# Performance work log

Measured on AMD Instinct MI355X. Metric: run time of the kernel, lower is better.

Reference implementation:

```python
import jax, jax.numpy as jnp
import numpy as np


def setup_inputs() -> dict:
    key = jax.random.key(0)
    kq, kk, kv, km = jax.random.split(key, 4)
    B, H, S, D = 8, 16, 1024, 64
    Q = jax.random.normal(kq, (B, H, S, D), dtype=jnp.float32)
    K = jax.random.normal(kk, (B, H, S, D), dtype=jnp.float32)
    V = jax.random.normal(kv, (B, H, S, D), dtype=jnp.float32)
    # True means masked, per torch masked_fill_ semantics
    attn_mask = jax.random.randint(km, (B, 1, S, S), 0, 2).astype(bool)
    return {"Q": Q, "K": K, "V": V, "attn_mask": attn_mask}


def reference(Q, K, V, attn_mask):
    # Attention(Q,K,V) = softmax(QK^T / sqrt(d_k)) V, with masked scores
    # set to 1e-9 (faithful to the original's masked_fill_(mask, 1e-09)).
    d_k = Q.shape[-1]
    scores = jnp.einsum('bhqd,bhkd->bhqk', Q, K) / jnp.sqrt(jnp.float32(d_k))
    scores = jnp.where(attn_mask, jnp.asarray(1e-9, scores.dtype), scores)
    attn = jax.nn.softmax(scores, axis=-1)          # [B,H,S,S]
    context = jnp.einsum('bhqk,bhkd->bhqd', attn, V)  # [B,H,S,D]
    return (context, attn)
```

## Files before the change

### kernel.cpp

```cpp
#include <hip/hip_runtime.h>
#include <hip/hip_bf16.h>

typedef __attribute__((ext_vector_type(4))) float f32x4;
typedef __attribute__((ext_vector_type(8))) short bf16x8;
typedef __attribute__((ext_vector_type(4))) int   i32x4;
typedef __attribute__((ext_vector_type(4))) unsigned u32x4;

#define S_LEN 1024
#define DQ    64
#define VSTR  266
#define PSTR  264
#define CSTR  68

__device__ __forceinline__ unsigned pk2(float a, float b) {
    union { __hip_bfloat162 h; unsigned u; } v;
    v.h = __float22bfloat162_rn(make_float2(a, b));
    return v.u;
}

__device__ __forceinline__ bf16x8 pack8(float4 a, float4 b) {
    union { bf16x8 v; unsigned u[4]; } r;
    r.u[0] = pk2(a.x, a.y); r.u[1] = pk2(a.z, a.w);
    r.u[2] = pk2(b.x, b.y); r.u[3] = pk2(b.z, b.w);
    return r.v;
}

__device__ __forceinline__ bf16x8 ld_frag2(const unsigned short* p) {
    union { bf16x8 v; unsigned u[4]; } r;
    r.u[0] = *(const unsigned*)(p);
    r.u[1] = *(const unsigned*)(p + 2);
    r.u[2] = *(const unsigned*)(p + 16);
    r.u[3] = *(const unsigned*)(p + 18);
    return r.v;
}

__device__ __forceinline__ float bflo(unsigned u) { union { unsigned x; float f; } v; v.x = u << 16;         return v.f; }
__device__ __forceinline__ float bfhi(unsigned u) { union { unsigned x; float f; } v; v.x = u & 0xffff0000u; return v.f; }

__global__ __launch_bounds__(256) void pack_mask(const int* __restrict__ Mg,
                                                 unsigned long long* __restrict__ Pk) {
    const int gw   = (int)((blockIdx.x * 256 + threadIdx.x) >> 6);
    const int lane = threadIdx.x & 63;
#pragma unroll 4
    for (int j = 0; j < 32; ++j) {
        const size_t g = ((size_t)gw * 32 + j) * 64 + lane;
        const int m = __builtin_nontemporal_load(Mg + g);
        const unsigned long long bal = __ballot(m != 0);
        if (lane == 0) Pk[(size_t)gw * 32 + j] = bal;
    }
}

template <int PACKED>
__global__ __launch_bounds__(1024, 8) void attn_fused(
    const float* __restrict__ Qg, const float* __restrict__ Kg,
    const float* __restrict__ Vg, const int* __restrict__ Mg,
    const unsigned* __restrict__ Mb,
    float* __restrict__ Og, float* __restrict__ Ag)
{
    const int tid  = threadIdx.x;
    const int lane = tid & 63;
    const int wid  = tid >> 6;
    const int l15  = lane & 15;
    const int lg   = lane >> 4;
    const int wc   = wid >> 1;
    const int wr   = wid & 1;

    const int raw  = blockIdx.x;
    const int xcd  = raw & 7;
    const int slot = raw >> 3;
    const int bh   = xcd * 16 + (slot >> 5);
    const int qt   = slot & 31;
    const int b    = bh >> 4;

    const size_t kvbase = (size_t)bh * (S_LEN * DQ);
    const float* Qp = Qg + kvbase + (size_t)qt * (32 * DQ);
    const float* Kp = Kg + kvbase;
    const float* Vp = Vg + kvbase;
    float*       Ap = Ag + (size_t)bh * (size_t)(S_LEN * S_LEN) + (size_t)(qt * 32) * S_LEN;
    float*       Op = Og + kvbase + (size_t)qt * (32 * DQ);

    __shared__ __align__(16) unsigned char smem[32 * PSTR * 2 + DQ * VSTR * 2];
    unsigned short* Pt  = (unsigned short*)smem;
    float*          red = (float*)smem;
    float*          Cx  = (float*)smem;
    unsigned short* Vt  = (unsigned short*)(smem + 32 * PSTR * 2);

    const int qrow = wr * 16 + l15;

    unsigned mwd[4];
    if (PACKED) {
        const unsigned* mw = Mb + ((size_t)b * S_LEN + qt * 32 + qrow) * 32 + wc;
#pragma unroll
        for (int i = 0; i < 4; ++i) mwd[i] = mw[i * 8];
    }

    bf16x8 aq0, aq1;
    {
        const float* qr = Qp + (size_t)qrow * DQ + lg * 4;
        aq0 = pack8(*(const float4*)(qr),      *(const float4*)(qr + 16));
        aq1 = pack8(*(const float4*)(qr + 32), *(const float4*)(qr + 48));
    }

    f32x4 sc[8];
#pragma unroll
    for (int t = 0; t < 8; ++t) sc[t] = (f32x4){0.f, 0.f, 0.f, 0.f};

#pragma unroll
    for (int i = 0; i < 4; ++i)
#pragma unroll
        for (int h = 0; h < 2; ++h) {
            const float* krow = Kp + (size_t)(i * 256 + wc * 32 + h * 16 + l15) * DQ + lg * 4;
            bf16x8 k0 = pack8(*(const float4*)(krow),      *(const float4*)(krow + 16));
            bf16x8 k1 = pack8(*(const float4*)(krow + 32), *(const float4*)(krow + 48));
            f32x4 acc = sc[i * 2 + h];
            acc = __builtin_amdgcn_mfma_f32_16x16x32_bf16(k0, aq0, acc, 0, 0, 0);
            acc = __builtin_amdgcn_mfma_f32_16x16x32_bf16(k1, aq1, acc, 0, 0, 0);
            sc[i * 2 + h] = acc;
        }

    if (PACKED) {
#pragma unroll
        for (int i = 0; i < 4; ++i)
#pragma unroll
            for (int h = 0; h < 2; ++h) {
                const int t = i * 2 + h;
#pragma unroll
                for (int r = 0; r < 4; ++r)
                    sc[t][r] = ((mwd[i] >> (h * 16 + lg * 4 + r)) & 1u) ? 1e-9f
                                                                        : sc[t][r] * 0.125f;
            }
    } else {
        const int* mrow = Mg + (size_t)b * (size_t)(S_LEN * S_LEN)
                        + (size_t)(qt * 32 + qrow) * S_LEN + wc * 32 + lg * 4;
#pragma unroll
        for (int i = 0; i < 4; ++i)
#pragma unroll
            for (int h = 0; h < 2; ++h) {
                const i32x4 m4 = *(const i32x4*)(mrow + i * 256 + h * 16);
                const int t = i * 2 + h;
#pragma unroll
                for (int r = 0; r < 4; ++r)
                    sc[t][r] = m4[r] ? 1e-9f : sc[t][r] * 0.125f;
            }
    }

    float rmax = sc[0][0];
#pragma unroll
    for (int t = 0; t < 8; ++t)
#pragma unroll
        for (int r = 0; r < 4; ++r) rmax = fmaxf(rmax, sc[t][r]);
    rmax = fmaxf(rmax, __shfl_xor(rmax, 16));
    rmax = fmaxf(rmax, __shfl_xor(rmax, 32));
    __syncthreads();
    if (lane < 16) red[qrow * 8 + wc] = rmax;
    __syncthreads();
    {
        const f32x4 a = *(const f32x4*)(red + qrow * 8);
        const f32x4 bq = *(const f32x4*)(red + qrow * 8 + 4);
        rmax = fmaxf(fmaxf(fmaxf(a[0], a[1]), fmaxf(a[2], a[3])),
                     fmaxf(fmaxf(bq[0], bq[1]), fmaxf(bq[2], bq[3])));
    }

    float rsum = 0.f;
#pragma unroll
    for (int t = 0; t < 8; ++t)
#pragma unroll
        for (int r = 0; r < 4; ++r) {
            const float p = __expf(sc[t][r] - rmax);
            sc[t][r] = p;
            rsum += p;
        }
    rsum += __shfl_xor(rsum, 16);
    rsum += __shfl_xor(rsum, 32);
    __syncthreads();
    if (lane < 16) red[qrow * 8 + wc] = rsum;
    __syncthreads();
    float rinv;
    {
        const f32x4 a = *(const f32x4*)(red + qrow * 8);
        const f32x4 bq = *(const f32x4*)(red + qrow * 8 + 4);
        rinv = 1.0f / ((a[0] + a[1] + a[2] + a[3]) + (bq[0] + bq[1] + bq[2] + bq[3]));
    }
#pragma unroll
    for (int t = 0; t < 8; ++t)
#pragma unroll
        for (int r = 0; r < 4; ++r) sc[t][r] *= rinv;

    bf16x8 paf[4];
#pragma unroll
    for (int i = 0; i < 4; ++i) {
        union { bf16x8 v; unsigned u[4]; } pa;
        pa.u[0] = pk2(sc[i * 2][0],     sc[i * 2][1]);
        pa.u[1] = pk2(sc[i * 2][2],     sc[i * 2][3]);
        pa.u[2] = pk2(sc[i * 2 + 1][0], sc[i * 2 + 1][1]);
        pa.u[3] = pk2(sc[i * 2 + 1][2], sc[i * 2 + 1][3]);
        paf[i] = pa.v;
    }

    f32x4 co[4];
#pragma unroll
    for (int m = 0; m < 4; ++m) co[m] = (f32x4){0.f, 0.f, 0.f, 0.f};

#pragma unroll
    for (int i = 0; i < 4; ++i) {
        __syncthreads();

        const float* vsrc = Vp + (size_t)i * (256 * DQ);
#pragma unroll
        for (int j = 0; j < 4; ++j) {
            const int f = (j * 1024 + tid) * 4;
            const float4 v4 = *(const float4*)(vsrc + f);
            const int k = f >> 6, d = f & 63;
            const unsigned u0 = pk2(v4.x, v4.y);
            const unsigned u1 = pk2(v4.z, v4.w);
            Vt[(d + 0) * VSTR + k] = (unsigned short)u0;
            Vt[(d + 1) * VSTR + k] = (unsigned short)(u0 >> 16);
            Vt[(d + 2) * VSTR + k] = (unsigned short)u1;
            Vt[(d + 3) * VSTR + k] = (unsigned short)(u1 >> 16);
        }

        {
            union { bf16x8 v; unsigned long long q[2]; } pa;
            pa.v = paf[i];
            unsigned short* prow = Pt + qrow * PSTR + wc * 32 + lg * 4;
            *(unsigned long long*)(prow)      = pa.q[0];
            *(unsigned long long*)(prow + 16) = pa.q[1];
        }
        __syncthreads();

        {
            const int row = tid >> 5, c8 = tid & 31;
            const u32x4 u = *(const u32x4*)(Pt + row * PSTR + c8 * 8);
            const f32x4 o0 = { bflo(u[0]), bfhi(u[0]), bflo(u[1]), bfhi(u[1]) };
            const f32x4 o1 = { bflo(u[2]), bfhi(u[2]), bflo(u[3]), bfhi(u[3]) };
            float* dst = Ap + (size_t)row * S_LEN + i * 256 + c8 * 8;
            __builtin_nontemporal_store(o0, (f32x4*)(dst));
            __builtin_nontemporal_store(o1, (f32x4*)(dst + 4));
        }

#pragma unroll
        for (int m = 0; m < 4; ++m) {
            const bf16x8 bv = ld_frag2(Vt + (size_t)(m * 16 + l15) * VSTR + wc * 32 + lg * 4);
            co[m] = __builtin_amdgcn_mfma_f32_16x16x32_bf16(paf[i], bv, co[m], 0, 0, 0);
        }
    }

    __syncthreads();
#pragma unroll
    for (int w = 0; w < 8; ++w) {
        if (wc == w) {
#pragma unroll
            for (int m = 0; m < 4; ++m)
#pragma unroll
                for (int r = 0; r < 4; ++r) {
                    float* p = Cx + (size_t)(wr * 16 + lg * 4 + r) * CSTR + m * 16 + l15;
                    if (w == 0) *p = co[m][r];
                    else        *p += co[m][r];
                }
        }
        __syncthreads();
    }

    if (tid < 512) {
        const int row = tid >> 4, col = (tid & 15) * 4;
        const f32x4 o = *(const f32x4*)(Cx + (size_t)row * CSTR + col);
        __builtin_nontemporal_store(o, (f32x4*)(Op + (size_t)row * DQ + col));
    }
}

extern "C" void kernel_launch(void* const* d_in, const int* in_sizes, int n_in,
                              void* d_out, int out_size, void* d_ws, size_t ws_size,
                              hipStream_t stream) {
    const float* Q = (const float*)d_in[0];
    const float* K = (const float*)d_in[1];
    const float* V = (const float*)d_in[2];
    const int*   M = (const int*)d_in[3];
    float* ctx  = (float*)d_out;
    float* attn = ctx + (size_t)8 * 16 * 1024 * 64;

    const size_t packed_bytes = (size_t)8 * 1024 * 1024 / 8;
    if (ws_size >= packed_bytes) {
        pack_mask<<<dim3(1024), dim3(256), 0, stream>>>(M, (unsigned long long*)d_ws);
        attn_fused<1><<<dim3(4096), dim3(1024), 0, stream>>>(
            Q, K, V, M, (const unsigned*)d_ws, ctx, attn);
    } else {
        attn_fused<0><<<dim3(4096), dim3(1024), 0, stream>>>(
            Q, K, V, M, nullptr, ctx, attn);
    }
}
```

Measured before the change: 399.5 us.

## Halve query tile to 16 rows, prefetch K/V in registers, tree-reduce context

Shrinks each block to 16 query rows with 8 waves (512 threads) and doubles the grid. K fragments are double-buffered in registers, and V chunks are prefetched before the softmax and between iterations, so global loads overlap compute. The serialized 8-step shared-memory context accumulation becomes a single write-then-sum reduction, and V fragments load as 64-bit reads with a new padding stride. The cost is that K and V are reloaded twice as often across blocks and register pressure rises.

```diff
diff --git a/kernel.cpp b/kernel.cpp
--- a/kernel.cpp
+++ b/kernel.cpp
@@ -8,9 +8,12 @@
 
 #define S_LEN 1024
 #define DQ    64
-#define VSTR  266
+#define QTL   16
+#define VSTR  268
 #define PSTR  264
 #define CSTR  68
+#define PT_BYTES (QTL * PSTR * 2)
+#define VT_BYTES (DQ * VSTR * 2)
 
 __device__ __forceinline__ unsigned pk2(float a, float b) {
     union { __hip_bfloat162 h; unsigned u; } v;
@@ -25,12 +28,10 @@
     return r.v;
 }
 
-__device__ __forceinline__ bf16x8 ld_frag2(const unsigned short* p) {
-    union { bf16x8 v; unsigned u[4]; } r;
-    r.u[0] = *(const unsigned*)(p);
-    r.u[1] = *(const unsigned*)(p + 2);
-    r.u[2] = *(const unsigned*)(p + 16);
-    r.u[3] = *(const unsigned*)(p + 18);
+__device__ __forceinline__ bf16x8 ld_frag64(const unsigned short* p) {
+    union { bf16x8 v; unsigned long long q[2]; } r;
+    r.q[0] = *(const unsigned long long*)(p);
+    r.q[1] = *(const unsigned long long*)(p + 16);
     return r.v;
 }
 
@@ -51,7 +52,7 @@
 }
 
 template <int PACKED>
-__global__ __launch_bounds__(1024, 8) void attn_fused(
+__global__ __launch_bounds__(512, 6) void attn_fused(
     const float* __restrict__ Qg, const float* __restrict__ Kg,
     const float* __restrict__ Vg, const int* __restrict__ Mg,
     const unsigned* __restrict__ Mb,
@@ -59,37 +60,36 @@
 {
     const int tid  = threadIdx.x;
     const int lane = tid & 63;
-    const int wid  = tid >> 6;
+    const int wc   = tid >> 6;
     const int l15  = lane & 15;
     const int lg   = lane >> 4;
-    const int wc   = wid >> 1;
-    const int wr   = wid & 1;
 
     const int raw  = blockIdx.x;
     const int xcd  = raw & 7;
     const int slot = raw >> 3;
-    const int bh   = xcd * 16 + (slot >> 5);
-    const int qt   = slot & 31;
+    const int bh   = xcd * 16 + (slot >> 6);
+    const int qt   = slot & 63;
     const int b    = bh >> 4;
 
     const size_t kvbase = (size_t)bh * (S_LEN * DQ);
-    const float* Qp = Qg + kvbase + (size_t)qt * (32 * DQ);
+    const float* Qp = Qg + kvbase + (size_t)qt * (QTL * DQ);
     const float* Kp = Kg + kvbase;
     const float* Vp = Vg + kvbase;
-    float*       Ap = Ag + (size_t)bh * (size_t)(S_LEN * S_LEN) + (size_t)(qt * 32) * S_LEN;
-    float*       Op = Og + kvbase + (size_t)qt * (32 * DQ);
-
-    __shared__ __align__(16) unsigned char smem[32 * PSTR * 2 + DQ * VSTR * 2];
+    float*       Ap = Ag + (size_t)bh * (size_t)(S_LEN * S_LEN) + (size_t)(qt * QTL) * S_LEN;
+    float*       Op = Og + kvbase + (size_t)qt * (QTL * DQ);
+
+    __shared__ __align__(16) unsigned char smem[PT_BYTES + VT_BYTES];
     unsigned short* Pt  = (unsigned short*)smem;
     float*          red = (float*)smem;
     float*          Cx  = (float*)smem;
-    unsigned short* Vt  = (unsigned short*)(smem + 32 * PSTR * 2);
-
-    const int qrow = wr * 16 + l15;
+    unsigned short* Vt  = (unsigned short*)(smem + PT_BYTES);
+    float*          Tt  = (float*)(smem + PT_BYTES);
+
+    const int qrow = l15;
 
     unsigned mwd[4];
     if (PACKED) {
-        const unsigned* mw = Mb + ((size_t)b * S_LEN + qt * 32 + qrow) * 32 + wc;
+        const unsigned* mw = Mb + ((size_t)b * S_LEN + qt * QTL + qrow) * 32 + wc;
 #pragma unroll
         for (int i = 0; i < 4; ++i) mwd[i] = mw[i * 8];
     }
@@ -105,18 +105,26 @@
 #pragma unroll
     for (int t = 0; t < 8; ++t) sc[t] = (f32x4){0.f, 0.f, 0.f, 0.f};
 
-#pragma unroll
-    for (int i = 0; i < 4; ++i)
-#pragma unroll
-        for (int h = 0; h < 2; ++h) {
-            const float* krow = Kp + (size_t)(i * 256 + wc * 32 + h * 16 + l15) * DQ + lg * 4;
-            bf16x8 k0 = pack8(*(const float4*)(krow),      *(const float4*)(krow + 16));
-            bf16x8 k1 = pack8(*(const float4*)(krow + 32), *(const float4*)(krow + 48));
-            f32x4 acc = sc[i * 2 + h];
-            acc = __builtin_amdgcn_mfma_f32_16x16x32_bf16(k0, aq0, acc, 0, 0, 0);
-            acc = __builtin_amdgcn_mfma_f32_16x16x32_bf16(k1, aq1, acc, 0, 0, 0);
-            sc[i * 2 + h] = acc;
-        }
+    float4 kb[2][4];
+    {
+        const float* kr0 = Kp + (size_t)(wc * 32 + l15) * DQ + lg * 4;
+        kb[0][0] = *(const float4*)(kr0);      kb[0][1] = *(const float4*)(kr0 + 16);
+        kb[0][2] = *(const float4*)(kr0 + 32); kb[0][3] = *(const float4*)(kr0 + 48);
+    }
+#pragma unroll
+    for (int s = 0; s < 8; ++s) {
+        const int cur = s & 1;
+        if (s < 7) {
+            const int sn = s + 1;
+            const float* kr = Kp + (size_t)((sn >> 1) * 256 + wc * 32 + (sn & 1) * 16 + l15) * DQ + lg * 4;
+            kb[cur ^ 1][0] = *(const float4*)(kr);      kb[cur ^ 1][1] = *(const float4*)(kr + 16);
+            kb[cur ^ 1][2] = *(const float4*)(kr + 32); kb[cur ^ 1][3] = *(const float4*)(kr + 48);
+        }
+        const bf16x8 k0 = pack8(kb[cur][0], kb[cur][1]);
+        const bf16x8 k1 = pack8(kb[cur][2], kb[cur][3]);
+        sc[s] = __builtin_amdgcn_mfma_f32_16x16x32_bf16(k0, aq0, sc[s], 0, 0, 0);
+        sc[s] = __builtin_amdgcn_mfma_f32_16x16x32_bf16(k1, aq1, sc[s], 0, 0, 0);
+    }
 
     if (PACKED) {
 #pragma unroll
@@ -131,7 +139,7 @@
             }
     } else {
         const int* mrow = Mg + (size_t)b * (size_t)(S_LEN * S_LEN)
-                        + (size_t)(qt * 32 + qrow) * S_LEN + wc * 32 + lg * 4;
+                        + (size_t)(qt * QTL + qrow) * S_LEN + wc * 32 + lg * 4;
 #pragma unroll
         for (int i = 0; i < 4; ++i)
 #pragma unroll
@@ -143,6 +151,11 @@
                     sc[t][r] = m4[r] ? 1e-9f : sc[t][r] * 0.125f;
             }
     }
+
+    float4 vbA[4];
+#pragma unroll
+    for (int j = 0; j < 4; ++j)
+        vbA[j] = *(const float4*)(Vp + (size_t)(j * 512 + tid) * 4);
 
     float rmax = sc[0][0];
 #pragma unroll
@@ -196,6 +209,7 @@
         pa.u[3] = pk2(sc[i * 2 + 1][2], sc[i * 2 + 1][3]);
         paf[i] = pa.v;
     }
+    __syncthreads();
 
     f32x4 co[4];
 #pragma unroll
@@ -203,13 +217,15 @@
 
 #pragma unroll
     for (int i = 0; i < 4; ++i) {
-        __syncthreads();
-
-        const float* vsrc = Vp + (size_t)i * (256 * DQ);
-#pragma unroll
-        for (int j = 0; j < 4; ++j) {
-            const int f = (j * 1024 + tid) * 4;
-            const float4 v4 = *(const float4*)(vsrc + f);
+        float4 vbB[4];
+#pragma unroll
+        for (int j = 0; j < 4; ++j)
+            vbB[j] = *(const float4*)(Vp + (size_t)i * (256 * DQ) + (size_t)((j + 4) * 512 + tid) * 4);
+
+#pragma unroll
+        for (int j = 0; j < 8; ++j) {
+            const float4 v4 = (j < 4) ? vbA[j & 3] : vbB[j & 3];
+            const int f = (j * 512 + tid) * 4;
             const int k = f >> 6, d = f & 63;
             const unsigned u0 = pk2(v4.x, v4.y);
             const unsigned u1 = pk2(v4.z, v4.w);
@@ -240,28 +256,42 @@
 
 #pragma unroll
         for (int m = 0; m < 4; ++m) {
-            const bf16x8 bv = ld_frag2(Vt + (size_t)(m * 16 + l15) * VSTR + wc * 32 + lg * 4);
+            const bf16x8 bv = ld_frag64(Vt + (size_t)(m * 16 + l15) * VSTR + wc * 32 + lg * 4);
             co[m] = __builtin_amdgcn_mfma_f32_16x16x32_bf16(paf[i], bv, co[m], 0, 0, 0);
         }
-    }
-
-    __syncthreads();
-#pragma unroll
-    for (int w = 0; w < 8; ++w) {
-        if (wc == w) {
-#pragma unroll
-            for (int m = 0; m < 4; ++m)
-#pragma unroll
-                for (int r = 0; r < 4; ++r) {
-                    float* p = Cx + (size_t)(wr * 16 + lg * 4 + r) * CSTR + m * 16 + l15;
-                    if (w == 0) *p = co[m][r];
-                    else        *p += co[m][r];
-                }
+
+        if (i < 3) {
+#pragma unroll
+            for (int j = 0; j < 4; ++j)
+                vbA[j] = *(const float4*)(Vp + (size_t)(i + 1) * (256 * DQ) + (size_t)(j * 512 + tid) * 4);
         }
         __syncthreads();
     }
 
-    if (tid < 512) {
+    if (wc > 0) {
+        float* T = Tt + (size_t)(wc - 1) * (QTL * CSTR);
+#pragma unroll
+        for (int m = 0; m < 4; ++m)
+#pragma unroll
+            for (int r = 0; r < 4; ++r)
+                T[(lg * 4 + r) * CSTR + m * 16 + l15] = co[m][r];
+    }
+    __syncthreads();
+    if (wc == 0) {
+#pragma unroll
+        for (int m = 0; m < 4; ++m)
+#pragma unroll
+            for (int r = 0; r < 4; ++r) {
+                float acc = co[m][r];
+#pragma unroll
+                for (int s = 0; s < 7; ++s)
+                    acc += Tt[(size_t)s * (QTL * CSTR) + (lg * 4 + r) * CSTR + m * 16 + l15];
+                Cx[(lg * 4 + r) * CSTR + m * 16 + l15] = acc;
+            }
+    }
+    __syncthreads();
+
+    if (tid < 256) {
         const int row = tid >> 4, col = (tid & 15) * 4;
         const f32x4 o = *(const f32x4*)(Cx + (size_t)row * CSTR + col);
         __builtin_nontemporal_store(o, (f32x4*)(Op + (size_t)row * DQ + col));
@@ -281,10 +311,10 @@
     const size_t packed_bytes = (size_t)8 * 1024 * 1024 / 8;
     if (ws_size >= packed_bytes) {
         pack_mask<<<dim3(1024), dim3(256), 0, stream>>>(M, (unsigned long long*)d_ws);
-        attn_fused<1><<<dim3(4096), dim3(1024), 0, stream>>>(
+        attn_fused<1><<<dim3(8192), dim3(512), 0, stream>>>(
             Q, K, V, M, (const unsigned*)d_ws, ctx, attn);
     } else {
-        attn_fused<0><<<dim3(4096), dim3(1024), 0, stream>>>(
+        attn_fused<0><<<dim3(8192), dim3(512), 0, stream>>>(
             Q, K, V, M, nullptr, ctx, attn);
     }
 }
```

Result: slower. 414.1 us (+3.6%).
